# Kernel tuning notes

Hardware: AMD Instinct MI355X
Metric: run time of the kernel (lower is better)

## Reference

```python
import jax, jax.numpy as jnp
import numpy as np

T, B, I, H, O = 256, 64, 512, 1024, 256


def setup_inputs() -> dict:
    key = jax.random.key(0)
    ks = jax.random.split(key, 7)
    s_ih = 1.0 / np.sqrt(H)
    return {
        "x": jax.random.normal(ks[0], (T, B, I), dtype=jnp.float32),
        "W_ih": jax.random.uniform(ks[1], (4 * H, I), dtype=jnp.float32, minval=-s_ih, maxval=s_ih),
        "W_hh": jax.random.uniform(ks[2], (4 * H, H), dtype=jnp.float32, minval=-s_ih, maxval=s_ih),
        "b_ih": jax.random.uniform(ks[3], (4 * H,), dtype=jnp.float32, minval=-s_ih, maxval=s_ih),
        "b_hh": jax.random.uniform(ks[4], (4 * H,), dtype=jnp.float32, minval=-s_ih, maxval=s_ih),
        "fc_W": jax.random.uniform(ks[5], (O, H), dtype=jnp.float32, minval=-s_ih, maxval=s_ih),
        "fc_b": jax.random.uniform(ks[6], (O,), dtype=jnp.float32, minval=-s_ih, maxval=s_ih),
    }


def _lstm(x, W_ih, W_hh, b_ih, b_hh):
    # x: (T, B, I) seq-first, as PyTorch default. Gate order: i, f, g, o.
    Bsz = x.shape[1]
    Hh = W_hh.shape[1]
    # precompute input projections for all time steps: (T, B, 4H)
    xz = jnp.einsum('tbi,gi->tbg', x, W_ih) + b_ih + b_hh

    def step(carry, xz_t):
        h, c = carry
        z = xz_t + h @ W_hh.T  # (B, 4H)
        i, f, g, o = jnp.split(z, 4, axis=-1)
        i = jax.nn.sigmoid(i)
        f = jax.nn.sigmoid(f)
        g = jnp.tanh(g)
        o = jax.nn.sigmoid(o)
        c = f * c + i * g
        h = o * jnp.tanh(c)
        return (h, c), h

    h0 = jnp.zeros((Bsz, Hh), dtype=x.dtype)
    c0 = jnp.zeros((Bsz, Hh), dtype=x.dtype)
    _, hs = jax.lax.scan(step, (h0, c0), xz)
    return hs  # (T, B, H)


def reference(x, W_ih, W_hh, b_ih, b_hh, fc_W, fc_b):
    out = _lstm(x, W_ih, W_hh, b_ih, b_hh)  # (T, B, H)
    # Faithful to original: out[:, -1, :] indexes the LAST BATCH element
    # (seq-first layout), giving (T, H), then fc -> (T, O).
    last = out[:, -1, :]
    return last @ fc_W.T + fc_b
```

## Files before the change

kernel.cpp:

```cpp
#include <hip/hip_runtime.h>
#include <hip/hip_bf16.h>
#include <stdint.h>

#define T_STEPS 256
#define BATCH   64
#define IN_DIM  512
#define HID     1024
#define OUT_DIM 256
#define G4      4096
#define SENT32  0x7FC07FC0u
#define SENT64  0x7FC07FC07FC07FC0ULL

__device__ __forceinline__ float bfbits2f(uint32_t b16) {
    return __uint_as_float(b16 << 16);
}
__device__ __forceinline__ uint32_t f2bfbits(float f) {
    uint32_t u = __float_as_uint(f);
    u += 0x7fffu + ((u >> 16) & 1u);
    return u >> 16;
}
__device__ __forceinline__ float fast_sigmoid(float x) {
    return 1.f / (1.f + __expf(-x));
}
__device__ __forceinline__ float fast_tanh(float x) {
    return 2.f / (1.f + __expf(-2.f * x)) - 1.f;
}
__device__ __forceinline__ bool any_sent(uint64_t v) {
    uint64_t x = v ^ SENT64;
    return (((x - 0x0001000100010001ULL) & ~x) & 0x8000800080008000ULL) != 0ULL;
}
__device__ __forceinline__ uint64_t poll_load(const uint64_t* p) {
    return __hip_atomic_load(p, __ATOMIC_RELAXED, __HIP_MEMORY_SCOPE_AGENT);
}

__global__ void init_sent(uint32_t* __restrict__ p, int n) {
    int i = blockIdx.x * 256 + threadIdx.x;
    if (i < n) p[i] = SENT32;
}

template<bool ABF16>
__global__ __launch_bounds__(256) void gemm_bt(
    const void* __restrict__ Av, long lda,
    const float* __restrict__ Bw, int ldb,
    const float* __restrict__ bias1,
    float* __restrict__ C, int ldc, int K)
{
    __shared__ float a_lds[64][68];
    __shared__ float w_lds[64][65];
    const int tid = threadIdx.x;
    const int m0 = blockIdx.y * 64, n0 = blockIdx.x * 64;
    const int kl = tid & 63, grp = tid >> 6;
    const int cc = tid & 31, r0 = (tid >> 5) * 8;

    float acc[16];
#pragma unroll
    for (int i = 0; i < 16; ++i) acc[i] = 0.f;

    for (int k0 = 0; k0 < K; k0 += 64) {
        __syncthreads();
#pragma unroll
        for (int i = 0; i < 16; ++i) {
            int r = grp + 4 * i;
            long ai = (long)(m0 + r) * lda + k0 + kl;
            float av = ABF16 ? bfbits2f(((const uint16_t*)Av)[ai])
                             : ((const float*)Av)[ai];
            a_lds[kl][r] = av;
            w_lds[kl][r] = Bw[(long)(n0 + r) * ldb + k0 + kl];
        }
        __syncthreads();
#pragma unroll 16
        for (int k = 0; k < 64; ++k) {
            float4 A0 = *(const float4*)&a_lds[k][r0];
            float4 A1 = *(const float4*)&a_lds[k][r0 + 4];
            float w0 = w_lds[k][cc], w1 = w_lds[k][cc + 32];
            float a[8] = {A0.x, A0.y, A0.z, A0.w, A1.x, A1.y, A1.z, A1.w};
#pragma unroll
            for (int i = 0; i < 8; ++i) {
                acc[i]     += a[i] * w0;
                acc[8 + i] += a[i] * w1;
            }
        }
    }
    float b0 = bias1[n0 + cc], b1 = bias1[n0 + cc + 32];
#pragma unroll
    for (int i = 0; i < 8; ++i) {
        C[(long)(m0 + r0 + i) * ldc + n0 + cc]      = acc[i]     + b0;
        C[(long)(m0 + r0 + i) * ldc + n0 + cc + 32] = acc[8 + i] + b1;
    }
}

__global__ __launch_bounds__(256, 1) void lstm_rec(
    const float* __restrict__ W_hh,
    const float* __restrict__ x,
    const float* __restrict__ W_ih,
    const float* __restrict__ b_ih,
    const float* __restrict__ b_hh,
    uint64_t* __restrict__ h_all)
{
    __shared__ float h_lds[2][HID];
    __shared__ float xz_lds[16][T_STEPS + 1];
    __shared__ float z_lds[16];

    const int g     = blockIdx.x;
    const int tid   = threadIdx.x;
    const int kpart = tid & 15;
    const int row   = tid >> 4;
    const int gate  = row >> 2;
    const int ju    = row & 3;
    const int grow  = gate * HID + g * 4 + ju;

    {
        float wih[32];
        const float* wp = W_ih + (long)grow * IN_DIM + kpart * 32;
#pragma unroll
        for (int i = 0; i < 8; ++i) {
            float4 v = *(const float4*)(wp + 4 * i);
            wih[4*i] = v.x; wih[4*i+1] = v.y; wih[4*i+2] = v.z; wih[4*i+3] = v.w;
        }
        float bsum = b_ih[grow] + b_hh[grow];
        const float* xbase = x + (long)63 * IN_DIM + (long)kpart * 32;
#pragma unroll 2
        for (int t = 0; t < T_STEPS; ++t) {
            const float* xp = xbase + (long)t * BATCH * IN_DIM;
            float a0 = 0.f, a1 = 0.f, a2 = 0.f, a3 = 0.f;
#pragma unroll
            for (int i = 0; i < 8; ++i) {
                float4 v = *(const float4*)(xp + 4 * i);
                a0 += v.x * wih[4*i];   a1 += v.y * wih[4*i+1];
                a2 += v.z * wih[4*i+2]; a3 += v.w * wih[4*i+3];
            }
            float acc = (a0 + a1) + (a2 + a3);
            acc += __shfl_xor(acc, 1, 16);
            acc += __shfl_xor(acc, 2, 16);
            acc += __shfl_xor(acc, 4, 16);
            acc += __shfl_xor(acc, 8, 16);
            if (kpart == 0) xz_lds[row][t] = acc + bsum;
        }
    }

    float w[64];
#pragma unroll
    for (int i = 0; i < 16; ++i) {
        int ch = (i + kpart) & 15;
        float4 wv = *(const float4*)&W_hh[(long)grow * HID + kpart * 64 + ch * 4];
        w[4*i] = wv.x; w[4*i+1] = wv.y; w[4*i+2] = wv.z; w[4*i+3] = wv.w;
    }

    {
        float4 z4 = {0.f, 0.f, 0.f, 0.f};
        *(float4*)&h_lds[0][4 * tid] = z4;
    }
    __syncthreads();

    float c_state = 0.f;
    float xz_next = xz_lds[row][0];

    for (int t = 0; t < T_STEPS; ++t) {
        float* hb = h_lds[t & 1];
        if (t > 0) {
            const uint64_t* hsrc = h_all + (size_t)(t - 1) * 256;
            uint64_t v = poll_load(&hsrc[tid]);
            if (any_sent(v)) {
                uint64_t a = poll_load(&hsrc[tid]);
                uint64_t b = poll_load(&hsrc[tid]);
                for (;;) {
                    v = a; a = b; b = poll_load(&hsrc[tid]);
                    if (!any_sent(v)) break;
                }
            }
            float4 hv = { bfbits2f((uint32_t)( v        & 0xFFFFu)),
                          bfbits2f((uint32_t)((v >> 16) & 0xFFFFu)),
                          bfbits2f((uint32_t)((v >> 32) & 0xFFFFu)),
                          bfbits2f((uint32_t)((v >> 48) & 0xFFFFu)) };
            *(float4*)&hb[4 * tid] = hv;
        }
        __syncthreads();

        float xz_cur = xz_next;
        int tn = (t + 1 < T_STEPS) ? t + 1 : t;
        xz_next = xz_lds[row][tn];

        float a0 = 0.f, a1 = 0.f, a2 = 0.f, a3 = 0.f;
#pragma unroll
        for (int i = 0; i < 16; ++i) {
            float4 hv = *(const float4*)&hb[kpart * 64 + ((i + kpart) & 15) * 4];
            a0 += w[4*i]   * hv.x;
            a1 += w[4*i+1] * hv.y;
            a2 += w[4*i+2] * hv.z;
            a3 += w[4*i+3] * hv.w;
        }
        float sum = (a0 + a1) + (a2 + a3);
        sum += __shfl_xor(sum, 1, 16);
        sum += __shfl_xor(sum, 2, 16);
        sum += __shfl_xor(sum, 4, 16);
        sum += __shfl_xor(sum, 8, 16);
        if (kpart == 0) z_lds[row] = sum + xz_cur;
        __syncthreads();

        if (tid < 4) {
            float zi = z_lds[tid], zf = z_lds[4 + tid];
            float zg = z_lds[8 + tid], zo = z_lds[12 + tid];
            float ii = fast_sigmoid(zi);
            float ff = fast_sigmoid(zf);
            float gg = fast_tanh(zg);
            float oo = fast_sigmoid(zo);
            c_state = ff * c_state + ii * gg;
            float h = oo * fast_tanh(c_state);
            uint32_t hb16 = f2bfbits(h);
            uint32_t b1 = __shfl(hb16, 1, 64);
            uint32_t b2 = __shfl(hb16, 2, 64);
            uint32_t b3 = __shfl(hb16, 3, 64);
            if (tid == 0) {
                uint64_t dw = (uint64_t)(hb16 | (b1 << 16))
                            | ((uint64_t)(b2 | (b3 << 16)) << 32);
                __hip_atomic_store(&h_all[(size_t)t * 256 + g], dw,
                                   __ATOMIC_RELAXED, __HIP_MEMORY_SCOPE_AGENT);
            }
        }
    }
}

extern "C" void kernel_launch(void* const* d_in, const int* in_sizes, int n_in,
                              void* d_out, int out_size, void* d_ws, size_t ws_size,
                              hipStream_t stream) {
    const float* x    = (const float*)d_in[0];
    const float* W_ih = (const float*)d_in[1];
    const float* W_hh = (const float*)d_in[2];
    const float* b_ih = (const float*)d_in[3];
    const float* b_hh = (const float*)d_in[4];
    const float* fc_W = (const float*)d_in[5];
    const float* fc_b = (const float*)d_in[6];
    float* out = (float*)d_out;

    uint64_t* h_all = (uint64_t*)d_ws;

    init_sent<<<(T_STEPS * HID / 2 + 255) / 256, 256, 0, stream>>>(
        (uint32_t*)h_all, T_STEPS * HID / 2);

    lstm_rec<<<256, 256, 0, stream>>>(W_hh, x, W_ih, b_ih, b_hh, h_all);

    gemm_bt<true><<<dim3(OUT_DIM / 64, T_STEPS / 64), 256, 0, stream>>>(
        (const void*)h_all, HID, fc_W, HID, fc_b, out, OUT_DIM, HID);
}
```

Baseline: 1.232 ms.

## Halve persistent LSTM blocks to 128 with 8 hidden units per block

The recurrent kernel now runs 128 blocks of 512 threads, each owning 8 hidden units (32 gate rows) instead of 256 blocks of 4 units. This halves the number of producers each step's cross-block h exchange must wait on and doubles the payload per store. The input projection is reorganised so each wave reduces four gate rows across 64 lanes. Large dynamic shared memory is requested, likely to force one block per CU, and the W_hh slice is held in explicit float4 registers, which may pressure VGPRs at 512 threads.

```diff
diff --git a/kernel.cpp b/kernel.cpp
--- a/kernel.cpp
+++ b/kernel.cpp
@@ -89,7 +89,16 @@
     }
 }
 
-__global__ __launch_bounds__(256, 1) void lstm_rec(
+#define GROWX(RR) ((long)((RR) >> 3) * HID + 8 * g + ((RR) & 7))
+
+#define WINIT(I) { const int ch_ = ((I) + kpart) & 15; \
+    w##I = *(const float4*)(W_hh + wbase + ch_ * 4); }
+
+#define MACS(I) { const float4 hv_ = *(const float4*)(hb + hoff + (((I) + kpart) & 15) * 4); \
+    a0 = fmaf(w##I.x, hv_.x, a0); a1 = fmaf(w##I.y, hv_.y, a1); \
+    a2 = fmaf(w##I.z, hv_.z, a2); a3 = fmaf(w##I.w, hv_.w, a3); }
+
+__global__ __launch_bounds__(512, 2) void lstm_rec(
     const float* __restrict__ W_hh,
     const float* __restrict__ x,
     const float* __restrict__ W_ih,
@@ -98,58 +107,75 @@
     uint64_t* __restrict__ h_all)
 {
     __shared__ float h_lds[2][HID];
-    __shared__ float xz_lds[16][T_STEPS + 1];
-    __shared__ float z_lds[16];
-
-    const int g     = blockIdx.x;
-    const int tid   = threadIdx.x;
+    __shared__ float xz_lds[32][T_STEPS + 1];
+    __shared__ float z_lds[32];
+    extern __shared__ float dyn_pad[];
+
+    const int g   = blockIdx.x;
+    const int tid = threadIdx.x;
+
+    {
+        const int wv = tid >> 6;
+        const int ln = tid & 63;
+        const int rr0 = 4 * wv;
+        const long gr0 = GROWX(rr0), gr1 = GROWX(rr0 + 1),
+                   gr2 = GROWX(rr0 + 2), gr3 = GROWX(rr0 + 3);
+        const float4 p0a = *(const float4*)(W_ih + gr0 * IN_DIM + 8 * ln);
+        const float4 p0b = *(const float4*)(W_ih + gr0 * IN_DIM + 8 * ln + 4);
+        const float4 p1a = *(const float4*)(W_ih + gr1 * IN_DIM + 8 * ln);
+        const float4 p1b = *(const float4*)(W_ih + gr1 * IN_DIM + 8 * ln + 4);
+        const float4 p2a = *(const float4*)(W_ih + gr2 * IN_DIM + 8 * ln);
+        const float4 p2b = *(const float4*)(W_ih + gr2 * IN_DIM + 8 * ln + 4);
+        const float4 p3a = *(const float4*)(W_ih + gr3 * IN_DIM + 8 * ln);
+        const float4 p3b = *(const float4*)(W_ih + gr3 * IN_DIM + 8 * ln + 4);
+        const float bs0 = b_ih[gr0] + b_hh[gr0];
+        const float bs1 = b_ih[gr1] + b_hh[gr1];
+        const float bs2 = b_ih[gr2] + b_hh[gr2];
+        const float bs3 = b_ih[gr3] + b_hh[gr3];
+        for (int t = 0; t < T_STEPS; ++t) {
+            const float* xp = x + ((long)t * BATCH + 63) * IN_DIM + 8 * ln;
+            const float4 xa = *(const float4*)xp;
+            const float4 xb = *(const float4*)(xp + 4);
+            float s0 = xa.x*p0a.x + xa.y*p0a.y + xa.z*p0a.z + xa.w*p0a.w
+                     + xb.x*p0b.x + xb.y*p0b.y + xb.z*p0b.z + xb.w*p0b.w;
+            float s1 = xa.x*p1a.x + xa.y*p1a.y + xa.z*p1a.z + xa.w*p1a.w
+                     + xb.x*p1b.x + xb.y*p1b.y + xb.z*p1b.z + xb.w*p1b.w;
+            float s2 = xa.x*p2a.x + xa.y*p2a.y + xa.z*p2a.z + xa.w*p2a.w
+                     + xb.x*p2b.x + xb.y*p2b.y + xb.z*p2b.z + xb.w*p2b.w;
+            float s3 = xa.x*p3a.x + xa.y*p3a.y + xa.z*p3a.z + xa.w*p3a.w
+                     + xb.x*p3b.x + xb.y*p3b.y + xb.z*p3b.z + xb.w*p3b.w;
+#pragma unroll
+            for (int d = 1; d < 64; d <<= 1) {
+                s0 += __shfl_xor(s0, d, 64);
+                s1 += __shfl_xor(s1, d, 64);
+                s2 += __shfl_xor(s2, d, 64);
+                s3 += __shfl_xor(s3, d, 64);
+            }
+            if (ln == 0) {
+                xz_lds[rr0 + 0][t] = s0 + bs0;
+                xz_lds[rr0 + 1][t] = s1 + bs1;
+                xz_lds[rr0 + 2][t] = s2 + bs2;
+                xz_lds[rr0 + 3][t] = s3 + bs3;
+            }
+        }
+    }
+
+    if (tid < 256) {
+        float4 z4 = {0.f, 0.f, 0.f, 0.f};
+        *(float4*)&h_lds[0][4 * tid] = z4;
+    }
+
     const int kpart = tid & 15;
     const int row   = tid >> 4;
-    const int gate  = row >> 2;
-    const int ju    = row & 3;
-    const int grow  = gate * HID + g * 4 + ju;
-
-    {
-        float wih[32];
-        const float* wp = W_ih + (long)grow * IN_DIM + kpart * 32;
-#pragma unroll
-        for (int i = 0; i < 8; ++i) {
-            float4 v = *(const float4*)(wp + 4 * i);
-            wih[4*i] = v.x; wih[4*i+1] = v.y; wih[4*i+2] = v.z; wih[4*i+3] = v.w;
-        }
-        float bsum = b_ih[grow] + b_hh[grow];
-        const float* xbase = x + (long)63 * IN_DIM + (long)kpart * 32;
-#pragma unroll 2
-        for (int t = 0; t < T_STEPS; ++t) {
-            const float* xp = xbase + (long)t * BATCH * IN_DIM;
-            float a0 = 0.f, a1 = 0.f, a2 = 0.f, a3 = 0.f;
-#pragma unroll
-            for (int i = 0; i < 8; ++i) {
-                float4 v = *(const float4*)(xp + 4 * i);
-                a0 += v.x * wih[4*i];   a1 += v.y * wih[4*i+1];
-                a2 += v.z * wih[4*i+2]; a3 += v.w * wih[4*i+3];
-            }
-            float acc = (a0 + a1) + (a2 + a3);
-            acc += __shfl_xor(acc, 1, 16);
-            acc += __shfl_xor(acc, 2, 16);
-            acc += __shfl_xor(acc, 4, 16);
-            acc += __shfl_xor(acc, 8, 16);
-            if (kpart == 0) xz_lds[row][t] = acc + bsum;
-        }
-    }
-
-    float w[64];
-#pragma unroll
-    for (int i = 0; i < 16; ++i) {
-        int ch = (i + kpart) & 15;
-        float4 wv = *(const float4*)&W_hh[(long)grow * HID + kpart * 64 + ch * 4];
-        w[4*i] = wv.x; w[4*i+1] = wv.y; w[4*i+2] = wv.z; w[4*i+3] = wv.w;
-    }
-
-    {
-        float4 z4 = {0.f, 0.f, 0.f, 0.f};
-        *(float4*)&h_lds[0][4 * tid] = z4;
-    }
+    const long grow  = GROWX(row);
+    const long wbase = grow * HID + kpart * 64;
+    const int  hoff  = kpart * 64;
+    float4 w0, w1, w2, w3, w4, w5, w6, w7, w8, w9, w10, w11, w12, w13, w14, w15;
+    WINIT(0)  WINIT(1)  WINIT(2)  WINIT(3)
+    WINIT(4)  WINIT(5)  WINIT(6)  WINIT(7)
+    WINIT(8)  WINIT(9)  WINIT(10) WINIT(11)
+    WINIT(12) WINIT(13) WINIT(14) WINIT(15)
+
     __syncthreads();
 
     float c_state = 0.f;
@@ -157,38 +183,42 @@
 
     for (int t = 0; t < T_STEPS; ++t) {
         float* hb = h_lds[t & 1];
-        if (t > 0) {
-            const uint64_t* hsrc = h_all + (size_t)(t - 1) * 256;
-            uint64_t v = poll_load(&hsrc[tid]);
-            if (any_sent(v)) {
-                uint64_t a = poll_load(&hsrc[tid]);
-                uint64_t b = poll_load(&hsrc[tid]);
+        if (t > 0 && tid < 128) {
+            const uint64_t* src = h_all + (size_t)(t - 1) * 256 + 2 * tid;
+            uint64_t v0 = poll_load(src), v1 = poll_load(src + 1);
+            if (any_sent(v0) | any_sent(v1)) {
+                uint64_t a0_ = poll_load(src), a1_ = poll_load(src + 1);
+                uint64_t b0_ = poll_load(src), b1_ = poll_load(src + 1);
                 for (;;) {
-                    v = a; a = b; b = poll_load(&hsrc[tid]);
-                    if (!any_sent(v)) break;
+                    uint64_t c0_ = poll_load(src), c1_ = poll_load(src + 1);
+                    if (!(any_sent(v0) | any_sent(v1))) break;
+                    v0 = a0_; v1 = a1_;
+                    a0_ = b0_; a1_ = b1_;
+                    b0_ = c0_; b1_ = c1_;
                 }
             }
-            float4 hv = { bfbits2f((uint32_t)( v        & 0xFFFFu)),
-                          bfbits2f((uint32_t)((v >> 16) & 0xFFFFu)),
-                          bfbits2f((uint32_t)((v >> 32) & 0xFFFFu)),
-                          bfbits2f((uint32_t)((v >> 48) & 0xFFFFu)) };
-            *(float4*)&hb[4 * tid] = hv;
-        }
-        __syncthreads();
-
-        float xz_cur = xz_next;
-        int tn = (t + 1 < T_STEPS) ? t + 1 : t;
+            float4 f0 = { bfbits2f((uint32_t)( v0        & 0xFFFFu)),
+                          bfbits2f((uint32_t)((v0 >> 16) & 0xFFFFu)),
+                          bfbits2f((uint32_t)((v0 >> 32) & 0xFFFFu)),
+                          bfbits2f((uint32_t)((v0 >> 48) & 0xFFFFu)) };
+            float4 f1 = { bfbits2f((uint32_t)( v1        & 0xFFFFu)),
+                          bfbits2f((uint32_t)((v1 >> 16) & 0xFFFFu)),
+                          bfbits2f((uint32_t)((v1 >> 32) & 0xFFFFu)),
+                          bfbits2f((uint32_t)((v1 >> 48) & 0xFFFFu)) };
+            *(float4*)&hb[8 * tid]     = f0;
+            *(float4*)&hb[8 * tid + 4] = f1;
+        }
+        __syncthreads();
+
+        const float xz_cur = xz_next;
+        const int tn = (t + 1 < T_STEPS) ? t + 1 : t;
         xz_next = xz_lds[row][tn];
 
         float a0 = 0.f, a1 = 0.f, a2 = 0.f, a3 = 0.f;
-#pragma unroll
-        for (int i = 0; i < 16; ++i) {
-            float4 hv = *(const float4*)&hb[kpart * 64 + ((i + kpart) & 15) * 4];
-            a0 += w[4*i]   * hv.x;
-            a1 += w[4*i+1] * hv.y;
-            a2 += w[4*i+2] * hv.z;
-            a3 += w[4*i+3] * hv.w;
-        }
+        MACS(0)  MACS(1)  MACS(2)  MACS(3)
+        MACS(4)  MACS(5)  MACS(6)  MACS(7)
+        MACS(8)  MACS(9)  MACS(10) MACS(11)
+        MACS(12) MACS(13) MACS(14) MACS(15)
         float sum = (a0 + a1) + (a2 + a3);
         sum += __shfl_xor(sum, 1, 16);
         sum += __shfl_xor(sum, 2, 16);
@@ -197,27 +227,28 @@
         if (kpart == 0) z_lds[row] = sum + xz_cur;
         __syncthreads();
 
-        if (tid < 4) {
-            float zi = z_lds[tid], zf = z_lds[4 + tid];
-            float zg = z_lds[8 + tid], zo = z_lds[12 + tid];
-            float ii = fast_sigmoid(zi);
-            float ff = fast_sigmoid(zf);
-            float gg = fast_tanh(zg);
-            float oo = fast_sigmoid(zo);
+        if (tid < 8) {
+            const float zi = z_lds[tid],      zf = z_lds[8 + tid];
+            const float zg = z_lds[16 + tid], zo = z_lds[24 + tid];
+            const float ii = fast_sigmoid(zi);
+            const float ff = fast_sigmoid(zf);
+            const float gg = fast_tanh(zg);
+            const float oo = fast_sigmoid(zo);
             c_state = ff * c_state + ii * gg;
-            float h = oo * fast_tanh(c_state);
-            uint32_t hb16 = f2bfbits(h);
-            uint32_t b1 = __shfl(hb16, 1, 64);
-            uint32_t b2 = __shfl(hb16, 2, 64);
-            uint32_t b3 = __shfl(hb16, 3, 64);
+            const float h = oo * fast_tanh(c_state);
+            uint32_t hbv = f2bfbits(h);
+            uint32_t lo  = hbv | (__shfl_down(hbv, 1, 64) << 16);
+            uint64_t A = (uint64_t)lo | ((uint64_t)__shfl(lo, 2, 64) << 32);
+            uint64_t B = (uint64_t)__shfl(lo, 4, 64)
+                       | ((uint64_t)__shfl(lo, 6, 64) << 32);
             if (tid == 0) {
-                uint64_t dw = (uint64_t)(hb16 | (b1 << 16))
-                            | ((uint64_t)(b2 | (b3 << 16)) << 32);
-                __hip_atomic_store(&h_all[(size_t)t * 256 + g], dw,
-                                   __ATOMIC_RELAXED, __HIP_MEMORY_SCOPE_AGENT);
-            }
-        }
-    }
+                uint64_t* dst = h_all + (size_t)t * 256 + 2 * g;
+                __hip_atomic_store(dst,     A, __ATOMIC_RELAXED, __HIP_MEMORY_SCOPE_AGENT);
+                __hip_atomic_store(dst + 1, B, __ATOMIC_RELAXED, __HIP_MEMORY_SCOPE_AGENT);
+            }
+        }
+    }
+    (void)dyn_pad;
 }
 
 extern "C" void kernel_launch(void* const* d_in, const int* in_sizes, int n_in,
@@ -234,10 +265,9 @@
 
     uint64_t* h_all = (uint64_t*)d_ws;
 
-    init_sent<<<(T_STEPS * HID / 2 + 255) / 256, 256, 0, stream>>>(
-        (uint32_t*)h_all, T_STEPS * HID / 2);
-
-    lstm_rec<<<256, 256, 0, stream>>>(W_hh, x, W_ih, b_ih, b_hh, h_all);
+    init_sent<<<512, 256, 0, stream>>>((uint32_t*)h_all, T_STEPS * HID / 2);
+
+    lstm_rec<<<128, 512, 41984, stream>>>(W_hh, x, W_ih, b_ih, b_hh, h_all);
 
     gemm_bt<true><<<dim3(OUT_DIM / 64, T_STEPS / 64), 256, 0, stream>>>(
         (const void*)h_all, HID, fc_W, HID, fc_b, out, OUT_DIM, HID);
```

Result: faster. 1.142 ms (-7.3%).
